# Performance work log

Hardware: AMD Instinct MI355X
Metric: run time of the kernel (lower is better)

Reference implementation:

```python
import jax, jax.numpy as jnp
import numpy as np

HIDDEN = 1280
NUM_HEADS = 16
HEAD_DIM = HIDDEN // NUM_HEADS  # 80
ROPE_DIM = HEAD_DIM // 2        # 40
THETA = 10000.0
SEQ = 3072


def setup_inputs() -> dict:
    key = jax.random.key(0)
    ks = jax.random.split(key, 6)
    hidden_states = jax.random.normal(ks[0], (SEQ, HIDDEN), dtype=jnp.float32)
    position_ids = jax.random.randint(ks[1], (SEQ, 2), 0, 64, dtype=jnp.int32)
    qkv_w = jax.random.normal(ks[2], (HIDDEN, 3 * HIDDEN), dtype=jnp.float32) * (HIDDEN ** -0.5)
    qkv_b = jax.random.normal(ks[3], (3 * HIDDEN,), dtype=jnp.float32) * 0.02
    o_w = jax.random.normal(ks[4], (HIDDEN, HIDDEN), dtype=jnp.float32) * (HIDDEN ** -0.5)
    o_b = jax.random.normal(ks[5], (HIDDEN,), dtype=jnp.float32) * 0.02
    return {"hidden_states": hidden_states, "position_ids": position_ids,
            "qkv_w": qkv_w, "qkv_b": qkv_b, "o_w": o_w, "o_b": o_b}


def _rotate_half(x):
    x1, x2 = jnp.split(x, 2, axis=-1)
    return jnp.concatenate([-x2, x1], axis=-1)


def reference(hidden_states, position_ids, qkv_w, qkv_b, o_w, o_b):
    seq_len = hidden_states.shape[0]
    # fused QKV projection
    qkv = hidden_states @ qkv_w + qkv_b                     # (S, 3*H*D)
    qkv = qkv.reshape(seq_len, 3, NUM_HEADS, HEAD_DIM)
    q, k, v = qkv[:, 0], qkv[:, 1], qkv[:, 2]               # each (S, h, d)
    # 2D RoPE: inv_freq over rope dim = head_dim // 2
    inv_freq = 1.0 / (THETA ** (jnp.arange(0, ROPE_DIM, 2, dtype=jnp.float32) / ROPE_DIM))
    pos = position_ids.astype(jnp.float32)
    h_freqs = jnp.outer(pos[:, 0], inv_freq)                # (S, rope/2)
    w_freqs = jnp.outer(pos[:, 1], inv_freq)                # (S, rope/2)
    freqs = jnp.concatenate([h_freqs, w_freqs], axis=-1)    # (S, rope)
    emb = jnp.concatenate([freqs, freqs], axis=-1)          # (S, head_dim)
    cos = jnp.cos(emb)[:, None, :]                          # (S, 1, d)
    sin = jnp.sin(emb)[:, None, :]
    q = q * cos + _rotate_half(q) * sin
    k = k * cos + _rotate_half(k) * sin
    # manual attention
    scaling = HEAD_DIM ** -0.5
    attn = jnp.einsum('qhd,khd->hqk', q * scaling, k)       # (h, S, S)
    attn = jax.nn.softmax(attn, axis=-1)
    out = jnp.einsum('hqk,khd->qhd', attn, v)               # (S, h, d)
    out = out.reshape(seq_len, HIDDEN)
    return out @ o_w + o_b
```

## Files before the change

kernel.cpp:

```cpp
#include <hip/hip_runtime.h>

#define SEQ  3072
#define HID  1280
#define NH   16
#define HD   80
#define NQKV 3840
#define KSP  2

typedef unsigned short u16;
typedef unsigned int u32;
typedef __attribute__((ext_vector_type(8))) short short8;
typedef __attribute__((ext_vector_type(4))) short short4v;
typedef __attribute__((ext_vector_type(4))) float floatx4;
typedef __attribute__((ext_vector_type(4))) unsigned int uint4v;

__device__ __forceinline__ u16 f2bf(float x) {
    u32 u = __float_as_uint(x);
    u += 0x7fffu + ((u >> 16) & 1u);
    return (u16)(u >> 16);
}
__device__ __forceinline__ u32 packrne(float a, float b) {
    return (u32)f2bf(a) | ((u32)f2bf(b) << 16);
}

typedef const __attribute__((address_space(1))) unsigned int* gp1_t;
typedef __attribute__((address_space(3))) unsigned int* lp3_t;
__device__ __forceinline__ void gld16(const void* g, void* l) {
    __builtin_amdgcn_global_load_lds((gp1_t)g, (lp3_t)l, 16, 0, 0);
}

__device__ __forceinline__ int swz80(int c, int r) {
    return (c < 8) ? (c ^ (r & 7)) : (8 + ((c - 8) ^ ((r >> 2) & 1)));
}

__global__ void prep_k(const int* __restrict__ pos, float* __restrict__ cosb,
                       float* __restrict__ sinb, const float* __restrict__ hs,
                       u16* __restrict__ hH, const float* __restrict__ qkvw,
                       u16* __restrict__ wT, const float* __restrict__ ow,
                       u16* __restrict__ owT) {
    __shared__ float tile[32][33];
    const int b = blockIdx.x, t = threadIdx.x;
    if (b < 480) {
        int i = b * 256 + t;
        int s = i / 40, j = i % 40;
        float p = (float)((j < 20) ? pos[s * 2] : pos[s * 2 + 1]);
        int k = (j < 20) ? j : j - 20;
        float inv = powf(10000.0f, -(float)k / 20.0f);
        float a = p * inv;
        cosb[s * 40 + j] = cosf(a);
        sinb[s * 40 + j] = sinf(a);
    } else if (b < 4320) {
        int i = (b - 480) * 256 + t;
        const float4 x = ((const float4*)hs)[i];
        uint2 o;
        o.x = packrne(x.x, x.y);
        o.y = packrne(x.z, x.w);
        ((uint2*)hH)[i] = o;
    } else {
        const float* w;
        u16* dst;
        int K, N, nx, ky;
        if (b < 9120) {
            int i = b - 4320;
            nx = i % 120; ky = i / 120; w = qkvw; dst = wT; K = HID; N = NQKV;
        } else {
            int i = b - 9120;
            nx = i % 40; ky = i / 40; w = ow; dst = owT; K = HID; N = HID;
        }
        int n0 = nx * 32, k0 = ky * 32;
        int c = t & 31, r8 = t >> 5;
        for (int rr = r8; rr < 32; rr += 8)
            tile[rr][c] = w[(size_t)(k0 + rr) * N + n0 + c];
        __syncthreads();
        for (int rr = r8; rr < 32; rr += 8)
            dst[(size_t)(n0 + rr) * K + k0 + c] = f2bf(tile[c][rr]);
    }
}

template<int BM, int BN>
__global__ __launch_bounds__(256, 3) void gemm_bf16_k(
    const u16* __restrict__ A, const u16* __restrict__ B,
    const float* __restrict__ bias, float* __restrict__ C,
    int M, int N, int K, int mode) {
    constexpr int GA = BM / 32;
    constexpr int GB = BN / 32;
    constexpr int FM = BM / 32;
    constexpr int FN = BN / 32;
    __shared__ u16 lA[BM * 64], lB[BN * 64];
    const int t = threadIdx.x, lane = t & 63, w = t >> 6;
    const int qi = lane & 15, quad = lane >> 4;
    int id = blockIdx.x;
    int xcd = id & 7, sN = id >> 3;
    int m_idx, n_idx;
    if (mode == 0) {
        n_idx = (xcd & 1) * 15 + sN % 15;
        m_idx = (xcd >> 1) * 6 + sN / 15;
    } else {
        m_idx = xcd * 6 + sN / 20;
        n_idx = sN % 20;
    }
    const int m0 = m_idx * BM, n0 = n_idx * BN;
    const int wm = (w >> 1) * (BM / 2), wn = (w & 1) * (BN / 2);

    floatx4 acc[FM][FN];
    for (int mi = 0; mi < FM; mi++)
        for (int ni = 0; ni < FN; ni++) acc[mi][ni] = (floatx4){0.f, 0.f, 0.f, 0.f};

    const int rg = lane >> 3;
    const int ce = ((lane & 7) ^ rg) * 8;
    size_t gA[GA], gB[GB];
    for (int g = 0; g < GA; g++) {
        int row = w * (BM / 4) + g * 8 + rg;
        gA[g] = (size_t)(m0 + row) * K + ce;
    }
    for (int g = 0; g < GB; g++) {
        int row = w * (BN / 4) + g * 8 + rg;
        gB[g] = (size_t)(n0 + row) * K + ce;
    }

    for (int k0 = 0; k0 < K; k0 += 64) {
        for (int g = 0; g < GA; g++)
            gld16(A + gA[g] + k0, &lA[(w * (BM / 4) + g * 8) * 64]);
        for (int g = 0; g < GB; g++)
            gld16(B + gB[g] + k0, &lB[(w * (BN / 4) + g * 8) * 64]);
        __syncthreads();
        short8 af[FM][2], bf[FN][2];
        for (int mi = 0; mi < FM; mi++) {
            int row = wm + mi * 16 + qi;
            for (int kh = 0; kh < 2; kh++)
                af[mi][kh] = *(const short8*)&lA[row * 64 + (((kh * 4 + quad) ^ (row & 7)) << 3)];
        }
        for (int ni = 0; ni < FN; ni++) {
            int row = wn + ni * 16 + qi;
            for (int kh = 0; kh < 2; kh++)
                bf[ni][kh] = *(const short8*)&lB[row * 64 + (((kh * 4 + quad) ^ (row & 7)) << 3)];
        }
        for (int mi = 0; mi < FM; mi++)
            for (int ni = 0; ni < FN; ni++) {
                acc[mi][ni] = __builtin_amdgcn_mfma_f32_16x16x32_bf16(af[mi][0], bf[ni][0], acc[mi][ni], 0, 0, 0);
                acc[mi][ni] = __builtin_amdgcn_mfma_f32_16x16x32_bf16(af[mi][1], bf[ni][1], acc[mi][ni], 0, 0, 0);
            }
        __syncthreads();
    }
    for (int mi = 0; mi < FM; mi++)
        for (int ni = 0; ni < FN; ni++) {
            int col = n0 + wn + ni * 16 + qi;
            int rowb = m0 + wm + mi * 16 + quad * 4;
            float b = bias[col];
            for (int r = 0; r < 4; r++)
                C[(size_t)(rowb + r) * N + col] = acc[mi][ni][r] + b;
        }
}

__global__ void pack_qkv_k(const float* __restrict__ qkv, const float* __restrict__ cosb,
                           const float* __restrict__ sinb,
                           u16* __restrict__ Qs, u16* __restrict__ Ks, u16* __restrict__ Vs) {
    __shared__ float lv[80 * 65];
    const int t = threadIdx.x;
    const int h = blockIdx.y, s0 = blockIdx.x * 64;
    const float qsc = 0.11180339887498949f * 1.4426950408889634f;

    for (int i = t; i < 64 * 10; i += 256) {
        int rl = i / 10, jg = i % 10;
        int s = s0 + rl, j = jg * 4;
        const float4 cc = *(const float4*)&cosb[s * 40 + j];
        const float4 ss = *(const float4*)&sinb[s * 40 + j];
        const float* qb = qkv + (size_t)s * NQKV + h * HD;
        const float4 q1 = *(const float4*)&qb[j];
        const float4 q2 = *(const float4*)&qb[j + 40];
        const float* kb = qb + HID;
        const float4 k1 = *(const float4*)&kb[j];
        const float4 k2 = *(const float4*)&kb[j + 40];
        uint2 qo1, qo2, ko1, ko2;
        qo1.x = packrne((q1.x * cc.x - q2.x * ss.x) * qsc, (q1.y * cc.y - q2.y * ss.y) * qsc);
        qo1.y = packrne((q1.z * cc.z - q2.z * ss.z) * qsc, (q1.w * cc.w - q2.w * ss.w) * qsc);
        qo2.x = packrne((q2.x * cc.x + q1.x * ss.x) * qsc, (q2.y * cc.y + q1.y * ss.y) * qsc);
        qo2.y = packrne((q2.z * cc.z + q1.z * ss.z) * qsc, (q2.w * cc.w + q1.w * ss.w) * qsc);
        ko1.x = packrne(k1.x * cc.x - k2.x * ss.x, k1.y * cc.y - k2.y * ss.y);
        ko1.y = packrne(k1.z * cc.z - k2.z * ss.z, k1.w * cc.w - k2.w * ss.w);
        ko2.x = packrne(k2.x * cc.x + k1.x * ss.x, k2.y * cc.y + k1.y * ss.y);
        ko2.y = packrne(k2.z * cc.z + k1.z * ss.z, k2.w * cc.w + k1.w * ss.w);
        size_t base = (size_t)(h * SEQ + s) * 80;
        int sub0 = j & 7, sub1 = (j + 40) & 7;
        int p0 = swz80(j >> 3, s);
        int p1 = swz80((j + 40) >> 3, s);
        *(uint2*)&Qs[base + p0 * 8 + sub0] = qo1;
        *(uint2*)&Qs[base + p1 * 8 + sub1] = qo2;
        *(uint2*)&Ks[base + p0 * 8 + sub0] = ko1;
        *(uint2*)&Ks[base + p1 * 8 + sub1] = ko2;
    }
    for (int i = t; i < 64 * 80; i += 256) {
        int rl = i / 80, d = i % 80;
        lv[d * 65 + rl] = qkv[(size_t)(s0 + rl) * NQKV + 2 * HID + h * HD + d];
    }
    __syncthreads();
    for (int i = t; i < 80 * 16; i += 256) {
        int d = i / 16, g = i % 16;
        int c2l = g * 4;
        float v0 = lv[d * 65 + c2l], v1 = lv[d * 65 + c2l + 1];
        float v2 = lv[d * 65 + c2l + 2], v3 = lv[d * 65 + c2l + 3];
        int pc = (g >> 1) ^ (d & 7);
        uint2 o;
        o.x = packrne(v0, v1);
        o.y = packrne(v2, v3);
        *(uint2*)&Vs[((size_t)h * HD + d) * SEQ + s0 + pc * 8 + (g & 1) * 4] = o;
    }
}

__global__ __launch_bounds__(512, 6) void attn_k(
    const u16* __restrict__ Qs, const u16* __restrict__ Ks, const u16* __restrict__ Vs,
    float* __restrict__ Op, float* __restrict__ lp) {
    __shared__ u16 kbuf[2][5120];
    __shared__ u16 vbuf[2][5120];

    const int t = threadIdx.x, lane = t & 63, w = t >> 6;
    const int qi = lane & 15, quad = lane >> 4;
    const int h = blockIdx.y, q0 = blockIdx.x * 128, ksp = blockIdx.z;
    const int kc0 = ksp * (SEQ / 2);
    u16* const kflat = &kbuf[0][0];

    {
        const u16* Qt = Qs + (size_t)(h * SEQ + q0) * 80;
        for (int i = w; i < 20; i += 8)
            gld16(Qt + i * 512 + lane * 8, kflat + i * 512);
    }
    __syncthreads();
    short8 bq[3];
    {
        const u16* rb = &kflat[(w * 16 + qi) * 80];
        bq[0] = *(const short8*)&rb[(quad ^ (qi & 7)) << 3];
        bq[1] = *(const short8*)&rb[((4 + quad) ^ (qi & 7)) << 3];
        short4v t2 = *(const short4v*)&rb[((8 + ((quad >> 1) ^ ((qi >> 2) & 1))) << 3) + ((quad & 1) << 2)];
        bq[2] = (short8){t2.x, t2.y, t2.z, t2.w, 0, 0, 0, 0};
    }
    __syncthreads();

    float l_lane = 0.f;
    floatx4 acco[5];
    for (int dt = 0; dt < 5; dt++) acco[dt] = (floatx4){0.f, 0.f, 0.f, 0.f};

    auto stage = [&](int it, int buf) {
        int kc = kc0 + it * 64;
        const u16* Kt = Ks + (size_t)(h * SEQ + kc) * 80;
        for (int i = w; i < 10; i += 8)
            gld16(Kt + i * 512 + lane * 8, &kbuf[buf][i * 512]);
        const u16* Vt = Vs + (size_t)h * HD * SEQ + kc;
        for (int i = w; i < 10; i += 8) {
            int p16 = i * 64 + lane;
            int d = p16 >> 3, pc = p16 & 7;
            gld16(Vt + (size_t)d * SEQ + pc * 8, &vbuf[buf][i * 512]);
        }
    };
    stage(0, 0);
    __syncthreads();

    const int NT = (SEQ / 2) / 64;
    for (int it = 0; it < NT; it++) {
        int cur = it & 1;
        if (it + 1 < NT) stage(it + 1, cur ^ 1);
        const u16* kb = &kbuf[cur][0];
        const u16* vb = &vbuf[cur][0];
#pragma unroll
        for (int c2 = 0; c2 < 2; c2++) {
            u32 pkx[2], pky[2];
#pragma unroll
            for (int ktl = 0; ktl < 2; ktl++) {
                int arow = (c2 * 2 + ktl) * 16 + qi;
                const u16* rb = &kb[arow * 80];
                short8 a0 = *(const short8*)&rb[(quad ^ (qi & 7)) << 3];
                short8 a1 = *(const short8*)&rb[((4 + quad) ^ (qi & 7)) << 3];
                short4v a2v = *(const short4v*)&rb[((8 + ((quad >> 1) ^ ((qi >> 2) & 1))) << 3) + ((quad & 1) << 2)];
                short8 a2 = (short8){a2v.x, a2v.y, a2v.z, a2v.w, 0, 0, 0, 0};
                floatx4 s = (floatx4){0.f, 0.f, 0.f, 0.f};
                __builtin_amdgcn_s_setprio(1);
                s = __builtin_amdgcn_mfma_f32_16x16x32_bf16(a0, bq[0], s, 0, 0, 0);
                s = __builtin_amdgcn_mfma_f32_16x16x32_bf16(a1, bq[1], s, 0, 0, 0);
                s = __builtin_amdgcn_mfma_f32_16x16x32_bf16(a2, bq[2], s, 0, 0, 0);
                __builtin_amdgcn_s_setprio(0);
                float e0 = __builtin_amdgcn_exp2f(s[0]);
                float e1 = __builtin_amdgcn_exp2f(s[1]);
                float e2 = __builtin_amdgcn_exp2f(s[2]);
                float e3 = __builtin_amdgcn_exp2f(s[3]);
                l_lane += (e0 + e1) + (e2 + e3);
                pkx[ktl] = __builtin_amdgcn_perm(__float_as_uint(e1), __float_as_uint(e0), 0x07060302u);
                pky[ktl] = __builtin_amdgcn_perm(__float_as_uint(e3), __float_as_uint(e2), 0x07060302u);
            }
            auto s0 = __builtin_amdgcn_permlane32_swap(pkx[0], pkx[1], false, false);
            auto s1 = __builtin_amdgcn_permlane32_swap(pky[0], pky[1], false, false);
            auto t0 = __builtin_amdgcn_permlane16_swap(s0[0], s0[1], false, false);
            auto t1 = __builtin_amdgcn_permlane16_swap(s1[0], s1[1], false, false);
            uint4v bb = (uint4v){t0[0], t1[0], t0[1], t1[1]};
            short8 bp = __builtin_bit_cast(short8, bb);
            int pv = (4 * c2 + quad) ^ (qi & 7);
            __builtin_amdgcn_s_setprio(1);
#pragma unroll
            for (int dt = 0; dt < 5; dt++) {
                short8 av = *(const short8*)&vb[((dt * 16 + qi) * 8 + pv) * 8];
                acco[dt] = __builtin_amdgcn_mfma_f32_16x16x32_bf16(av, bp, acco[dt], 0, 0, 0);
            }
            __builtin_amdgcn_s_setprio(0);
        }
        __syncthreads();
    }

    {
        float lq = l_lane;
        lq += __shfl_xor(lq, 16);
        lq += __shfl_xor(lq, 32);
        int q = q0 + w * 16 + qi;
        if (quad == 0) lp[(size_t)(ksp * NH + h) * SEQ + q] = lq;
        for (int dt = 0; dt < 5; dt++)
            for (int r = 0; r < 4; r++) {
                int d = dt * 16 + quad * 4 + r;
                Op[((size_t)(ksp * NH + h) * HD + d) * SEQ + q] = acco[dt][r];
            }
    }
}

__global__ void merge_k(const float* __restrict__ Op, const float* __restrict__ lp,
                        u16* __restrict__ att) {
    __shared__ float ls[HD * 65];
    __shared__ float li[64];
    const int t = threadIdx.x;
    const int h = blockIdx.y, q0 = blockIdx.x * 64;
    for (int i = t; i < HD * 16; i += 256) {
        int d = i / 16, g = i % 16;
        size_t a0 = ((size_t)h * HD + d) * SEQ + q0 + g * 4;
        size_t a1 = ((size_t)(NH + h) * HD + d) * SEQ + q0 + g * 4;
        const float4 v0 = *(const float4*)&Op[a0];
        const float4 v1 = *(const float4*)&Op[a1];
        ls[d * 65 + g * 4 + 0] = v0.x + v1.x;
        ls[d * 65 + g * 4 + 1] = v0.y + v1.y;
        ls[d * 65 + g * 4 + 2] = v0.z + v1.z;
        ls[d * 65 + g * 4 + 3] = v0.w + v1.w;
    }
    if (t < 64)
        li[t] = 1.0f / (lp[(size_t)h * SEQ + q0 + t] + lp[(size_t)(NH + h) * SEQ + q0 + t]);
    __syncthreads();
    for (int i = t; i < 64 * 40; i += 256) {
        int ql = i / 40, dg = i % 40;
        int d0 = dg * 2;
        float s = li[ql];
        u32 o = packrne(ls[d0 * 65 + ql] * s, ls[(d0 + 1) * 65 + ql] * s);
        *(u32*)&att[(size_t)(q0 + ql) * HID + h * HD + d0] = o;
    }
}

extern "C" void kernel_launch(void* const* d_in, const int* in_sizes, int n_in,
                              void* d_out, int out_size, void* d_ws, size_t ws_size,
                              hipStream_t stream) {
    const float* hs   = (const float*)d_in[0];
    const int*   pos  = (const int*)d_in[1];
    const float* qkvw = (const float*)d_in[2];
    const float* qkvb = (const float*)d_in[3];
    const float* ow   = (const float*)d_in[4];
    const float* ob   = (const float*)d_in[5];
    float* out = (float*)d_out;

    char* p = (char*)d_ws;
    auto alloc = [&](size_t bytes) {
        char* r = p;
        p += (bytes + 255) & ~(size_t)255;
        return r;
    };
    float* cosb = (float*)alloc((size_t)SEQ * 40 * 4);
    float* sinb = (float*)alloc((size_t)SEQ * 40 * 4);
    u16* owT = (u16*)alloc((size_t)HID * HID * 2);
    char* pool1 = alloc(7864320 + 9830400);
    u16* hH = (u16*)pool1;
    u16* wT = (u16*)(pool1 + 7864320);
    u16* Qs = (u16*)pool1;
    u16* Ks = (u16*)(pool1 + 7864320);
    char* pool2 = alloc((size_t)SEQ * NQKV * 4);
    float* qkv_s = (float*)pool2;
    u16* att  = (u16*)pool2;
    float* Op = (float*)(pool2 + 7864320);
    float* lp = (float*)(pool2 + 39321600);
    u16* Vs = (u16*)alloc((size_t)NH * HD * SEQ * 2);

    hipLaunchKernelGGL(prep_k, dim3(10720), dim3(256), 0, stream,
                       pos, cosb, sinb, hs, hH, qkvw, wT, ow, owT);
    hipLaunchKernelGGL((gemm_bf16_k<128, 128>), dim3(720), dim3(256), 0, stream,
                       hH, wT, qkvb, qkv_s, SEQ, NQKV, HID, 0);
    hipLaunchKernelGGL(pack_qkv_k, dim3(SEQ / 64, NH), dim3(256), 0, stream,
                       qkv_s, cosb, sinb, Qs, Ks, Vs);
    hipLaunchKernelGGL(attn_k, dim3(SEQ / 128, NH, 2), dim3(512), 0, stream,
                       Qs, Ks, Vs, Op, lp);
    hipLaunchKernelGGL(merge_k, dim3(SEQ / 64, NH), dim3(256), 0, stream, Op, lp, att);
    hipLaunchKernelGGL((gemm_bf16_k<64, 64>), dim3(960), dim3(256), 0, stream,
                       att, owT, ob, out, SEQ, HID, HID, 1);
}
```

Baseline: 229.7 us.

## Fuse RoPE, scaling and QKV packing into the QKV GEMM epilogue

Replaces the QKV GEMM plus separate pack_qkv kernel with a dedicated GEMM using 128x80 tiles, one head slice per tile. The epilogue adds bias, applies RoPE via lane shuffles with interleaved cos/sin, scales Q, and writes bf16 Q/K/V directly in the swizzled layouts attention expects. This removes the fp32 qkv intermediate write and re-read and one kernel launch. In exchange the epilogue does scattered 2-byte stores, and the 80-wide N tile gives a less regular MFMA shape; workspace buffers are also reorganized.

Measured after the change: 227.4 us. About the same (-1.0%).

```diff
diff --git a/kernel.cpp b/kernel.cpp
--- a/kernel.cpp
+++ b/kernel.cpp
@@ -33,8 +33,8 @@
     return (c < 8) ? (c ^ (r & 7)) : (8 + ((c - 8) ^ ((r >> 2) & 1)));
 }
 
-__global__ void prep_k(const int* __restrict__ pos, float* __restrict__ cosb,
-                       float* __restrict__ sinb, const float* __restrict__ hs,
+__global__ void prep_k(const int* __restrict__ pos, float2* __restrict__ csb,
+                       const float* __restrict__ hs,
                        u16* __restrict__ hH, const float* __restrict__ qkvw,
                        u16* __restrict__ wT, const float* __restrict__ ow,
                        u16* __restrict__ owT) {
@@ -47,8 +47,7 @@
         int k = (j < 20) ? j : j - 20;
         float inv = powf(10000.0f, -(float)k / 20.0f);
         float a = p * inv;
-        cosb[s * 40 + j] = cosf(a);
-        sinb[s * 40 + j] = sinf(a);
+        csb[s * 40 + j] = make_float2(cosf(a), sinf(a));
     } else if (b < 4320) {
         int i = (b - 480) * 256 + t;
         const float4 x = ((const float4*)hs)[i];
@@ -74,6 +73,132 @@
         __syncthreads();
         for (int rr = r8; rr < 32; rr += 8)
             dst[(size_t)(n0 + rr) * K + k0 + c] = f2bf(tile[c][rr]);
+    }
+}
+
+__global__ __launch_bounds__(256, 4) void gemm_qkv_k(
+    const u16* __restrict__ A, const u16* __restrict__ B,
+    const float* __restrict__ bias, const float2* __restrict__ csb,
+    u16* __restrict__ Qs, u16* __restrict__ Ks, u16* __restrict__ Vs) {
+    __shared__ u16 lA[128 * 64], lB[80 * 64];
+    const int t = threadIdx.x, lane = t & 63, w = t >> 6;
+    const int qi = lane & 15, quad = lane >> 4;
+    const int K = HID;
+    int id = blockIdx.x;
+    int xcd = id & 7, sN = id >> 3;
+    int m_idx = (xcd >> 1) * 6 + sN / 24;
+    int n_idx = (xcd & 1) * 24 + sN % 24;
+    const int m0 = m_idx * 128;
+    const int nb = n_idx * 80;
+
+    floatx4 acc[2][5];
+    for (int mi = 0; mi < 2; mi++)
+        for (int ni = 0; ni < 5; ni++) acc[mi][ni] = (floatx4){0.f, 0.f, 0.f, 0.f};
+
+    const int rg = lane >> 3;
+    const int ce = ((lane & 7) ^ rg) * 8;
+    size_t gA[4];
+    for (int j = 0; j < 4; j++) {
+        int row = m0 + (w * 4 + j) * 8 + rg;
+        gA[j] = (size_t)row * K + ce;
+    }
+    size_t gB[3];
+    int nB = 0;
+    for (int g = w; g < 10; g += 4) {
+        int row = nb + g * 8 + rg;
+        gB[nB++] = (size_t)row * K + ce;
+    }
+
+    for (int k0 = 0; k0 < K; k0 += 64) {
+        for (int j = 0; j < 4; j++)
+            gld16(A + gA[j] + k0, &lA[((w * 4 + j) * 8) * 64]);
+        {
+            int bi = 0;
+            for (int g = w; g < 10; g += 4)
+                gld16(B + gB[bi++] + k0, &lB[(g * 8) * 64]);
+        }
+        __syncthreads();
+        short8 af[2][2];
+        for (int mi = 0; mi < 2; mi++) {
+            int row = w * 32 + mi * 16 + qi;
+            for (int kh = 0; kh < 2; kh++)
+                af[mi][kh] = *(const short8*)&lA[row * 64 + (((kh * 4 + quad) ^ (row & 7)) << 3)];
+        }
+#pragma unroll
+        for (int ni = 0; ni < 5; ni++) {
+            int row = ni * 16 + qi;
+            short8 b0 = *(const short8*)&lB[row * 64 + ((quad ^ (row & 7)) << 3)];
+            short8 b1 = *(const short8*)&lB[row * 64 + (((4 + quad) ^ (row & 7)) << 3)];
+            for (int mi = 0; mi < 2; mi++) {
+                acc[mi][ni] = __builtin_amdgcn_mfma_f32_16x16x32_bf16(af[mi][0], b0, acc[mi][ni], 0, 0, 0);
+                acc[mi][ni] = __builtin_amdgcn_mfma_f32_16x16x32_bf16(af[mi][1], b1, acc[mi][ni], 0, 0, 0);
+            }
+        }
+        __syncthreads();
+    }
+
+    const int ht = n_idx >> 4;
+    const int h = n_idx & 15;
+    float bs[5];
+    for (int ni = 0; ni < 5; ni++)
+        bs[ni] = bias[ht * HID + h * HD + ni * 16 + qi];
+
+    if (ht == 2) {
+        for (int mi = 0; mi < 2; mi++) {
+            int s = m0 + w * 32 + mi * 16 + quad * 4;
+            int g = (s & 63) >> 2;
+            size_t base = (size_t)(s & ~63);
+            for (int ni = 0; ni < 5; ni++) {
+                int d = ni * 16 + qi;
+                uint2 o;
+                o.x = packrne(acc[mi][ni][0] + bs[ni], acc[mi][ni][1] + bs[ni]);
+                o.y = packrne(acc[mi][ni][2] + bs[ni], acc[mi][ni][3] + bs[ni]);
+                int pc = (g >> 1) ^ (d & 7);
+                *(uint2*)&Vs[((size_t)h * HD + d) * SEQ + base + pc * 8 + (g & 1) * 4] = o;
+            }
+        }
+    } else {
+        const float qsc = (ht == 0) ? 0.11180339887498949f * 1.4426950408889634f : 1.0f;
+        u16* dst = (ht == 0) ? Qs : Ks;
+        int dm[5];
+        dm[0] = qi;
+        dm[1] = 16 + qi;
+        dm[2] = (qi & 8) ? (qi - 8) : (32 + qi);
+        dm[3] = 8 + qi;
+        dm[4] = 24 + qi;
+        for (int mi = 0; mi < 2; mi++) {
+#pragma unroll
+            for (int r = 0; r < 4; r++) {
+                int s = m0 + w * 32 + mi * 16 + quad * 4 + r;
+                float val[5], sh[5];
+                for (int ni = 0; ni < 5; ni++) val[ni] = acc[mi][ni][r] + bs[ni];
+                for (int ni = 0; ni < 5; ni++) sh[ni] = __shfl_xor(val[ni], 8);
+                const float2* cr = csb + (size_t)s * 40;
+                float out[5];
+                {
+                    float2 c0 = cr[dm[0]];
+                    float p = (qi & 8) ? sh[3] : sh[2];
+                    out[0] = (val[0] * c0.x - p * c0.y) * qsc;
+                    float2 c1 = cr[dm[1]];
+                    p = (qi & 8) ? sh[4] : sh[3];
+                    out[1] = (val[1] * c1.x - p * c1.y) * qsc;
+                    float2 c2 = cr[dm[2]];
+                    if (qi & 8) out[2] = (val[2] * c2.x + sh[0] * c2.y) * qsc;
+                    else        out[2] = (val[2] * c2.x - sh[4] * c2.y) * qsc;
+                    float2 c3 = cr[dm[3]];
+                    p = (qi & 8) ? sh[1] : sh[0];
+                    out[3] = (val[3] * c3.x + p * c3.y) * qsc;
+                    float2 c4 = cr[dm[4]];
+                    p = (qi & 8) ? sh[2] : sh[1];
+                    out[4] = (val[4] * c4.x + p * c4.y) * qsc;
+                }
+                size_t rowb = (size_t)(h * SEQ + s) * 80;
+                for (int ni = 0; ni < 5; ni++) {
+                    int c = 2 * ni + (qi >> 3);
+                    dst[rowb + swz80(c, s) * 8 + (qi & 7)] = f2bf(out[ni]);
+                }
+            }
+        }
     }
 }
 
@@ -150,61 +275,6 @@
             for (int r = 0; r < 4; r++)
                 C[(size_t)(rowb + r) * N + col] = acc[mi][ni][r] + b;
         }
-}
-
-__global__ void pack_qkv_k(const float* __restrict__ qkv, const float* __restrict__ cosb,
-                           const float* __restrict__ sinb,
-                           u16* __restrict__ Qs, u16* __restrict__ Ks, u16* __restrict__ Vs) {
-    __shared__ float lv[80 * 65];
-    const int t = threadIdx.x;
-    const int h = blockIdx.y, s0 = blockIdx.x * 64;
-    const float qsc = 0.11180339887498949f * 1.4426950408889634f;
-
-    for (int i = t; i < 64 * 10; i += 256) {
-        int rl = i / 10, jg = i % 10;
-        int s = s0 + rl, j = jg * 4;
-        const float4 cc = *(const float4*)&cosb[s * 40 + j];
-        const float4 ss = *(const float4*)&sinb[s * 40 + j];
-        const float* qb = qkv + (size_t)s * NQKV + h * HD;
-        const float4 q1 = *(const float4*)&qb[j];
-        const float4 q2 = *(const float4*)&qb[j + 40];
-        const float* kb = qb + HID;
-        const float4 k1 = *(const float4*)&kb[j];
-        const float4 k2 = *(const float4*)&kb[j + 40];
-        uint2 qo1, qo2, ko1, ko2;
-        qo1.x = packrne((q1.x * cc.x - q2.x * ss.x) * qsc, (q1.y * cc.y - q2.y * ss.y) * qsc);
-        qo1.y = packrne((q1.z * cc.z - q2.z * ss.z) * qsc, (q1.w * cc.w - q2.w * ss.w) * qsc);
-        qo2.x = packrne((q2.x * cc.x + q1.x * ss.x) * qsc, (q2.y * cc.y + q1.y * ss.y) * qsc);
-        qo2.y = packrne((q2.z * cc.z + q1.z * ss.z) * qsc, (q2.w * cc.w + q1.w * ss.w) * qsc);
-        ko1.x = packrne(k1.x * cc.x - k2.x * ss.x, k1.y * cc.y - k2.y * ss.y);
-        ko1.y = packrne(k1.z * cc.z - k2.z * ss.z, k1.w * cc.w - k2.w * ss.w);
-        ko2.x = packrne(k2.x * cc.x + k1.x * ss.x, k2.y * cc.y + k1.y * ss.y);
-        ko2.y = packrne(k2.z * cc.z + k1.z * ss.z, k2.w * cc.w + k1.w * ss.w);
-        size_t base = (size_t)(h * SEQ + s) * 80;
-        int sub0 = j & 7, sub1 = (j + 40) & 7;
-        int p0 = swz80(j >> 3, s);
-        int p1 = swz80((j + 40) >> 3, s);
-        *(uint2*)&Qs[base + p0 * 8 + sub0] = qo1;
-        *(uint2*)&Qs[base + p1 * 8 + sub1] = qo2;
-        *(uint2*)&Ks[base + p0 * 8 + sub0] = ko1;
-        *(uint2*)&Ks[base + p1 * 8 + sub1] = ko2;
-    }
-    for (int i = t; i < 64 * 80; i += 256) {
-        int rl = i / 80, d = i % 80;
-        lv[d * 65 + rl] = qkv[(size_t)(s0 + rl) * NQKV + 2 * HID + h * HD + d];
-    }
-    __syncthreads();
-    for (int i = t; i < 80 * 16; i += 256) {
-        int d = i / 16, g = i % 16;
-        int c2l = g * 4;
-        float v0 = lv[d * 65 + c2l], v1 = lv[d * 65 + c2l + 1];
-        float v2 = lv[d * 65 + c2l + 2], v3 = lv[d * 65 + c2l + 3];
-        int pc = (g >> 1) ^ (d & 7);
-        uint2 o;
-        o.x = packrne(v0, v1);
-        o.y = packrne(v2, v3);
-        *(uint2*)&Vs[((size_t)h * HD + d) * SEQ + s0 + pc * 8 + (g & 1) * 4] = o;
-    }
 }
 
 __global__ __launch_bounds__(512, 6) void attn_k(
@@ -363,27 +433,22 @@
         p += (bytes + 255) & ~(size_t)255;
         return r;
     };
-    float* cosb = (float*)alloc((size_t)SEQ * 40 * 4);
-    float* sinb = (float*)alloc((size_t)SEQ * 40 * 4);
+    float2* csb = (float2*)alloc((size_t)SEQ * 40 * 8);
     u16* owT = (u16*)alloc((size_t)HID * HID * 2);
-    char* pool1 = alloc(7864320 + 9830400);
-    u16* hH = (u16*)pool1;
-    u16* wT = (u16*)(pool1 + 7864320);
-    u16* Qs = (u16*)pool1;
-    u16* Ks = (u16*)(pool1 + 7864320);
-    char* pool2 = alloc((size_t)SEQ * NQKV * 4);
-    float* qkv_s = (float*)pool2;
-    u16* att  = (u16*)pool2;
-    float* Op = (float*)(pool2 + 7864320);
-    float* lp = (float*)(pool2 + 39321600);
-    u16* Vs = (u16*)alloc((size_t)NH * HD * SEQ * 2);
+    u16* hH  = (u16*)alloc((size_t)SEQ * HID * 2);
+    u16* Qs  = (u16*)alloc((size_t)NH * SEQ * HD * 2);
+    u16* Ks  = (u16*)alloc((size_t)NH * SEQ * HD * 2);
+    u16* Vs  = (u16*)alloc((size_t)NH * SEQ * HD * 2);
+    char* poolB = alloc((size_t)KSP * NH * HD * SEQ * 4);
+    u16* wT = (u16*)poolB;
+    float* Op = (float*)poolB;
+    float* lp = (float*)alloc((size_t)KSP * NH * SEQ * 4);
+    u16* att = hH;
 
     hipLaunchKernelGGL(prep_k, dim3(10720), dim3(256), 0, stream,
-                       pos, cosb, sinb, hs, hH, qkvw, wT, ow, owT);
-    hipLaunchKernelGGL((gemm_bf16_k<128, 128>), dim3(720), dim3(256), 0, stream,
-                       hH, wT, qkvb, qkv_s, SEQ, NQKV, HID, 0);
-    hipLaunchKernelGGL(pack_qkv_k, dim3(SEQ / 64, NH), dim3(256), 0, stream,
-                       qkv_s, cosb, sinb, Qs, Ks, Vs);
+                       pos, csb, hs, hH, qkvw, wT, ow, owT);
+    hipLaunchKernelGGL(gemm_qkv_k, dim3(1152), dim3(256), 0, stream,
+                       hH, wT, qkvb, csb, Qs, Ks, Vs);
     hipLaunchKernelGGL(attn_k, dim3(SEQ / 128, NH, 2), dim3(512), 0, stream,
                        Qs, Ks, Vs, Op, lp);
     hipLaunchKernelGGL(merge_k, dim3(SEQ / 64, NH), dim3(256), 0, stream, Op, lp, att);
```
